# Kernel tuning notes

Hardware: AMD Instinct MI355X
Metric: run time of the kernel (lower is better)

## Reference

```python
import jax, jax.numpy as jnp
import numpy as np

ALPHA = 2.0  # spikingjelly ATan default

@jax.custom_vjp
def atan_spike(x):
    # Heaviside forward
    return (x >= 0).astype(x.dtype)

def _atan_fwd(x):
    return atan_spike(x), x

def _atan_bwd(x, g):
    c = (jnp.pi / 2.0) * ALPHA
    return (g * (ALPHA / 2.0) / (1.0 + (c * x) ** 2),)

atan_spike.defvjp(_atan_fwd, _atan_bwd)

def setup_inputs() -> dict:
    key = jax.random.key(0)
    k1, k2 = jax.random.split(key)
    T, B, N = 32, 128, 16384
    x_seq = jax.random.normal(k1, (T, B, N), dtype=jnp.float32)
    beta_raw = jnp.asarray(2.0, dtype=jnp.float32)  # _beta param; beta = sigmoid(_beta)
    return {"x_seq": x_seq, "beta_raw": beta_raw}

def reference(x_seq, beta_raw):
    beta = jax.nn.sigmoid(beta_raw)
    one = jnp.asarray(1.0, x_seq.dtype)

    def step(v, x_t):
        v = beta * v + x_t
        s = atan_spike(v - one)
        # hard reset, detach_reset=True
        v = v * (one - jax.lax.stop_gradient(s))
        return v, s

    v0 = jnp.zeros_like(x_seq[0])
    _, s_seq = jax.lax.scan(step, v0, x_seq)
    return s_seq
```

## Files before the change

kernel.cpp:

```cpp
#include <hip/hip_runtime.h>


#define T_STEPS 32
#define PF 4

typedef float vfloat4 __attribute__((ext_vector_type(4)));

__global__ __launch_bounds__(256) void plif_fwd_kernel(
    const vfloat4* __restrict__ x, const float* __restrict__ beta_raw,
    vfloat4* __restrict__ out, int bn4)
{
    int i = blockIdx.x * blockDim.x + threadIdx.x;
    if (i >= bn4) return;

    float beta = 1.0f / (1.0f + expf(-beta_raw[0]));

    vfloat4 v = (vfloat4)(0.0f, 0.0f, 0.0f, 0.0f);

    vfloat4 buf[PF];
    #pragma unroll
    for (int k = 0; k < PF; ++k) buf[k] = x[i + k * bn4];

    #pragma unroll
    for (int t = 0; t < T_STEPS; ++t) {
        vfloat4 xt = buf[t % PF];
        if (t + PF < T_STEPS)
            buf[t % PF] = x[i + (t + PF) * bn4];

        vfloat4 s;
        #pragma unroll
        for (int c = 0; c < 4; ++c) {
            v[c] = __fadd_rn(__fmul_rn(beta, v[c]), xt[c]);
            s[c] = (__fadd_rn(v[c], -1.0f) >= 0.0f) ? 1.0f : 0.0f;
            v[c] *= (1.0f - s[c]);
        }

        __builtin_nontemporal_store(s, &out[i + t * bn4]);
    }
}

extern "C" void kernel_launch(void* const* d_in, const int* in_sizes, int n_in,
                              void* d_out, int out_size, void* d_ws, size_t ws_size,
                              hipStream_t stream) {
    const float* x        = (const float*)d_in[0];
    const float* beta_raw = (const float*)d_in[1];
    float* out            = (float*)d_out;

    int total = in_sizes[0];
    int bn    = total / T_STEPS;
    int bn4   = bn / 4;

    dim3 block(256);
    dim3 grid((bn4 + block.x - 1) / block.x);
    plif_fwd_kernel<<<grid, block, 0, stream>>>(
        (const vfloat4*)x, beta_raw, (vfloat4*)out, bn4);
}
```

Measured before the change: 474.8 us.

## Double-buffer inline-asm vector loads in chunks of eight timesteps

Replaces the 4-deep rolling prefetch with two 8-entry register buffers filled by hand-written global_load_dwordx4 instructions. Explicit s_waitcnt vmcnt(8) and empty asm fences keep one chunk of loads in flight while the previous chunk is consumed, aiming to hide more memory latency per thread. It also adds a min-blocks-per-CU launch bound and drops the nontemporal store hint. Manual vmcnt accounting is fragile because stores share the counter, and the higher register use may reduce occupancy.

```diff
diff --git a/kernel.cpp b/kernel.cpp
--- a/kernel.cpp
+++ b/kernel.cpp
@@ -2,41 +2,66 @@
 
 
 #define T_STEPS 32
-#define PF 4
+#define CH 8
 
 typedef float vfloat4 __attribute__((ext_vector_type(4)));
 
-__global__ __launch_bounds__(256) void plif_fwd_kernel(
-    const vfloat4* __restrict__ x, const float* __restrict__ beta_raw,
+#define ISSUE(buf, tc)                                                        \
+    _Pragma("unroll")                                                         \
+    for (int k = 0; k < CH; ++k) {                                            \
+        unsigned voff = base16 + (unsigned)((tc) + k) * stride16;             \
+        asm volatile("global_load_dwordx4 %0, %1, %2"                        \
+                     : "=v"(buf[k])                                           \
+                     : "v"(voff), "s"(xp));                                   \
+    }
+
+#define WAIT8 asm volatile("s_waitcnt vmcnt(8)" ::: "memory")
+
+#define FENCE(buf)                                                            \
+    _Pragma("unroll")                                                         \
+    for (int k = 0; k < CH; ++k) asm volatile("" : "+v"(buf[k]));
+
+#define CONSUME(buf, tc)                                                      \
+    _Pragma("unroll")                                                         \
+    for (int k = 0; k < CH; ++k) {                                            \
+        vfloat4 xt = buf[k];                                                  \
+        vfloat4 s;                                                            \
+        _Pragma("unroll")                                                     \
+        for (int c = 0; c < 4; ++c) {                                         \
+               \
+            v[c] = __fadd_rn(__fmul_rn(beta, v[c]), xt[c]);                   \
+                                \
+            s[c] = (__fadd_rn(v[c], -1.0f) >= 0.0f) ? 1.0f : 0.0f;            \
+                                      \
+            v[c] *= (1.0f - s[c]);                                            \
+        }                                                                     \
+        out[i + ((tc) + k) * bn4] = s;                                        \
+    }
+
+__global__ __launch_bounds__(256, 4) void plif_fwd_kernel(
+    const vfloat4* __restrict__ xp, const float* __restrict__ beta_raw,
     vfloat4* __restrict__ out, int bn4)
 {
     int i = blockIdx.x * blockDim.x + threadIdx.x;
     if (i >= bn4) return;
 
     float beta = 1.0f / (1.0f + expf(-beta_raw[0]));
+    asm volatile("" : "+v"(beta));
+
+    unsigned base16   = (unsigned)i * 16u;
+    unsigned stride16 = (unsigned)bn4 * 16u;
 
     vfloat4 v = (vfloat4)(0.0f, 0.0f, 0.0f, 0.0f);
+    vfloat4 A[CH], B[CH];
 
-    vfloat4 buf[PF];
-    #pragma unroll
-    for (int k = 0; k < PF; ++k) buf[k] = x[i + k * bn4];
-
-    #pragma unroll
-    for (int t = 0; t < T_STEPS; ++t) {
-        vfloat4 xt = buf[t % PF];
-        if (t + PF < T_STEPS)
-            buf[t % PF] = x[i + (t + PF) * bn4];
-
-        vfloat4 s;
-        #pragma unroll
-        for (int c = 0; c < 4; ++c) {
-            v[c] = __fadd_rn(__fmul_rn(beta, v[c]), xt[c]);
-            s[c] = (__fadd_rn(v[c], -1.0f) >= 0.0f) ? 1.0f : 0.0f;
-            v[c] *= (1.0f - s[c]);
-        }
-
-        __builtin_nontemporal_store(s, &out[i + t * bn4]);
-    }
+    ISSUE(A, 0);
+    ISSUE(B, 8);
+    WAIT8; FENCE(A); CONSUME(A, 0);
+    ISSUE(A, 16);
+    WAIT8; FENCE(B); CONSUME(B, 8);
+    ISSUE(B, 24);
+    WAIT8; FENCE(A); CONSUME(A, 16);
+    WAIT8; FENCE(B); CONSUME(B, 24);
 }
 
 extern "C" void kernel_launch(void* const* d_in, const int* in_sizes, int n_in,
```

Result: faster. 456.1 us (-3.9%).
